# Kernel tuning notes

Measured on AMD Instinct MI355X. Metric: run time of the kernel, lower is better.

## Reference

```python
import jax, jax.numpy as jnp
import numpy as np
from jax import lax

B, T, H, E, V, ENC = 2048, 48, 512, 256, 128, 1024


def setup_inputs() -> dict:
    key = jax.random.key(0)
    ks = jax.random.split(key, 13)
    s = 0.05  # weight scale to keep activations sane
    return {
        "tgt_ids": jax.random.randint(ks[0], (B, T), 0, V),
        "enc_hid": jax.random.normal(ks[1], (B, ENC), jnp.float32),
        "W_init1": s * jax.random.normal(ks[2], (ENC, H), jnp.float32),
        "W_init2": s * jax.random.normal(ks[3], (ENC, H), jnp.float32),
        "embed_table": s * jax.random.normal(ks[4], (V, E), jnp.float32),
        "k1": s * jax.random.normal(ks[5], (E, 3 * H), jnp.float32),
        "rk1": s * jax.random.normal(ks[6], (H, 3 * H), jnp.float32),
        "b1": jnp.zeros((2, 3 * H), jnp.float32),
        "k2": s * jax.random.normal(ks[7], (H, 3 * H), jnp.float32),
        "rk2": s * jax.random.normal(ks[8], (H, 3 * H), jnp.float32),
        "b2": jnp.zeros((2, 3 * H), jnp.float32),
        "Wv": s * jax.random.normal(ks[9], (H, V), jnp.float32),
        "bv": jnp.zeros((V,), jnp.float32),
    }


def gru_masked(x_proj, mask, h0, rk, rb):
    """Keras GRU (reset_after=True, gate order z,r,h) with mask carry-through.
    x_proj: [B,T,3H] precomputed x@kernel + input_bias. mask: [B,T] bool.
    Masked steps keep previous state AND previous output (Keras masking semantics;
    GRU output == state)."""
    def step(h, inp):
        xg, m = inp  # xg: [B,3H], m: [B]
        inner = h @ rk + rb  # [B,3H]
        xz, xr, xh = jnp.split(xg, 3, axis=-1)
        rz, rr, rh = jnp.split(inner, 3, axis=-1)
        z = jax.nn.sigmoid(xz + rz)
        r = jax.nn.sigmoid(xr + rr)
        hh = jnp.tanh(xh + r * rh)
        h_new = z * h + (1.0 - z) * hh
        h = jnp.where(m[:, None], h_new, h)
        return h, h

    _, seq = lax.scan(step, h0, (x_proj.transpose(1, 0, 2), mask.T))
    return seq.transpose(1, 0, 2)  # [B,T,H]


def reference(tgt_ids, enc_hid, W_init1, W_init2, embed_table,
              k1, rk1, b1, k2, rk2, b2, Wv, bv):
    mask = tgt_ids != 0  # mask_zero=True
    emb = embed_table[tgt_ids]  # [B,T,E]
    h01 = enc_hid @ W_init1  # Dense no-bias init of layer-1 state
    h02 = enc_hid @ W_init2
    x1 = emb @ k1 + b1[0]  # [B,T,3H]
    seq1 = gru_masked(x1, mask, h01, rk1, b1[1])
    x2 = seq1 @ k2 + b2[0]
    seq2 = gru_masked(x2, mask, h02, rk2, b2[1])
    probs = jax.nn.softmax(seq2 @ Wv + bv, axis=-1)  # [B,T,V]
    return probs
```

## Files before the change

kernel.cpp:

```cpp
#include <hip/hip_runtime.h>
#include <hip/hip_bf16.h>
#include <math.h>

#define B_   2048
#define T_   48
#define H_   512
#define E_   256
#define V_   128
#define ENC_ 1024
#define H3_  1536
#define BH_  (B_ * H_)
#define NBLK_ 512

typedef __attribute__((ext_vector_type(8))) short bf16x8;
typedef __attribute__((ext_vector_type(4))) float f32x4;
typedef unsigned short ushort_t;

#if defined(__has_builtin)
#if __has_builtin(__builtin_amdgcn_global_load_lds)
#define HAVE_ASYNC 1
#endif
#endif
#ifndef HAVE_ASYNC
#define HAVE_ASYNC 0
#endif

__device__ __forceinline__ void stage16(const ushort_t* g, ushort_t* l, int lane)
{
#if HAVE_ASYNC
    __builtin_amdgcn_global_load_lds(
        (const __attribute__((address_space(1))) unsigned int*)g,
        (__attribute__((address_space(3))) unsigned int*)l, 16, 0, 0);
#else
    *(bf16x8*)(l + lane * 8) = *(const bf16x8*)g;
#endif
}

__device__ __forceinline__ float sigmoidf_(float x) { return 1.0f / (1.0f + expf(-x)); }

constexpr int BM = 64, BN = 64, BK = 16;

__global__ __launch_bounds__(256) void gemm_f32(
    const float* __restrict__ A, const float* __restrict__ Bm,
    const float* __restrict__ bias, float* __restrict__ C,
    int M, int N, int K)
{
    __shared__ float As[BK][BM + 4];
    __shared__ float Bs[BK][BN + 4];

    const int tid = threadIdx.x;
    const int bm = blockIdx.y * BM;
    const int bn = blockIdx.x * BN;
    const int tm = (tid >> 4) * 4;
    const int tn = (tid & 15) * 4;
    const int lmA = tid >> 2;
    const int lkA = (tid & 3) * 4;
    const int lkB = tid >> 4;
    const int lnB = (tid & 15) * 4;

    float acc[4][4] = {};

    for (int k0 = 0; k0 < K; k0 += BK) {
        float4 av  = *(const float4*)(A  + (size_t)(bm + lmA) * K + (k0 + lkA));
        float4 bv4 = *(const float4*)(Bm + (size_t)(k0 + lkB) * N + (bn + lnB));
        As[lkA + 0][lmA] = av.x;
        As[lkA + 1][lmA] = av.y;
        As[lkA + 2][lmA] = av.z;
        As[lkA + 3][lmA] = av.w;
        *(float4*)&Bs[lkB][lnB] = bv4;
        __syncthreads();

        #pragma unroll
        for (int k = 0; k < BK; ++k) {
            float4 a = *(const float4*)&As[k][tm];
            float4 b = *(const float4*)&Bs[k][tn];
            acc[0][0] += a.x * b.x; acc[0][1] += a.x * b.y; acc[0][2] += a.x * b.z; acc[0][3] += a.x * b.w;
            acc[1][0] += a.y * b.x; acc[1][1] += a.y * b.y; acc[1][2] += a.y * b.z; acc[1][3] += a.y * b.w;
            acc[2][0] += a.z * b.x; acc[2][1] += a.z * b.y; acc[2][2] += a.z * b.z; acc[2][3] += a.z * b.w;
            acc[3][0] += a.w * b.x; acc[3][1] += a.w * b.y; acc[3][2] += a.w * b.z; acc[3][3] += a.w * b.w;
        }
        __syncthreads();
    }

    #pragma unroll
    for (int r = 0; r < 4; ++r)
        #pragma unroll
        for (int c = 0; c < 4; ++c) {
            float v = acc[r][c];
            if (bias) v += bias[bn + tn + c];
            C[(size_t)(bm + tm + r) * N + (bn + tn + c)] = v;
        }
}

__global__ __launch_bounds__(256) void transpose_to_bf16(
    const float* __restrict__ W, __hip_bfloat16* __restrict__ Wt, int K, int N)
{
    __shared__ float tile[32][33];
    const int bk = blockIdx.y * 32, bn = blockIdx.x * 32;
    const int tx = threadIdx.x & 31, ty = threadIdx.x >> 5;
    #pragma unroll
    for (int i = ty; i < 32; i += 8)
        tile[i][tx] = W[(size_t)(bk + i) * N + (bn + tx)];
    __syncthreads();
    #pragma unroll
    for (int i = ty; i < 32; i += 8)
        Wt[(size_t)(bn + i) * K + (bk + tx)] = __float2bfloat16(tile[tx][i]);
}

__global__ __launch_bounds__(256) void transpose_split(
    const float* __restrict__ W, __hip_bfloat16* __restrict__ Whi,
    __hip_bfloat16* __restrict__ Wlo, int K, int N)
{
    __shared__ float tile[32][33];
    const int bk = blockIdx.y * 32, bn = blockIdx.x * 32;
    const int tx = threadIdx.x & 31, ty = threadIdx.x >> 5;
    #pragma unroll
    for (int i = ty; i < 32; i += 8)
        tile[i][tx] = W[(size_t)(bk + i) * N + (bn + tx)];
    __syncthreads();
    #pragma unroll
    for (int i = ty; i < 32; i += 8) {
        const float v = tile[tx][i];
        const __hip_bfloat16 h = __float2bfloat16(v);
        Whi[(size_t)(bn + i) * K + (bk + tx)] = h;
        Wlo[(size_t)(bn + i) * K + (bk + tx)] = __float2bfloat16(v - __bfloat162float(h));
    }
}

__global__ __launch_bounds__(256) void split_cast(
    const float* __restrict__ x, __hip_bfloat16* __restrict__ hi,
    __hip_bfloat16* __restrict__ lo, int n)
{
    const int i0 = (blockIdx.x * 256 + threadIdx.x) * 4;
    if (i0 >= n) return;
    const float4 v = *(const float4*)(x + i0);
    const float vv[4] = { v.x, v.y, v.z, v.w };
    #pragma unroll
    for (int j = 0; j < 4; ++j) {
        const __hip_bfloat16 h = __float2bfloat16(vv[j]);
        hi[i0 + j] = h;
        lo[i0 + j] = __float2bfloat16(vv[j] - __bfloat162float(h));
    }
}

__global__ __launch_bounds__(256, 2) void init_mfma(
    const ushort_t* __restrict__ ehi, const ushort_t* __restrict__ elo,
    const ushort_t* __restrict__ w1hi, const ushort_t* __restrict__ w1lo,
    const ushort_t* __restrict__ w2hi, const ushort_t* __restrict__ w2lo,
    float* __restrict__ h1f, __hip_bfloat16* __restrict__ h1b,
    float* __restrict__ h2f, __hip_bfloat16* __restrict__ h2b)
{
    const ushort_t* whi = blockIdx.z ? w2hi : w1hi;
    const ushort_t* wlo = blockIdx.z ? w2lo : w1lo;
    float* hf = blockIdx.z ? h2f : h1f;
    __hip_bfloat16* hb = blockIdx.z ? h2b : h1b;

    __shared__ __attribute__((aligned(16))) ushort_t Ahi[2][4096];
    __shared__ __attribute__((aligned(16))) ushort_t Alo[2][4096];
    __shared__ __attribute__((aligned(16))) ushort_t Bhi[2][2048];
    __shared__ __attribute__((aligned(16))) ushort_t Blo[2][2048];

    const int tid  = threadIdx.x;
    const int lane = tid & 63;
    const int w    = tid >> 6;
    const int ln   = lane & 15;
    const int kg   = lane >> 4;
    const int wr   = w >> 1, wc = w & 1;
    const int m0   = blockIdx.y * 64;
    const int i0   = blockIdx.x * 32;

    const int crow = lane >> 3;
    const int ckof = ((lane & 7) ^ crow) * 8;
    const int ko0 = (kg * 8) ^ ((ln & 7) * 8);
    const int ko1 = (32 + kg * 8) ^ ((ln & 7) * 8);

    auto STG = [&](int pb, int k0) {
        #pragma unroll
        for (int c = w; c < 24; c += 4) {
            const ushort_t* g; ushort_t* l;
            if (c < 8) {
                g = ehi + (size_t)(m0 + c * 8 + crow) * ENC_ + k0 + ckof;
                l = &Ahi[pb][c * 512];
            } else if (c < 16) {
                const int cc = c - 8;
                g = elo + (size_t)(m0 + cc * 8 + crow) * ENC_ + k0 + ckof;
                l = &Alo[pb][cc * 512];
            } else if (c < 20) {
                const int cc = c - 16;
                g = whi + (size_t)(i0 + cc * 8 + crow) * ENC_ + k0 + ckof;
                l = &Bhi[pb][cc * 512];
            } else {
                const int cc = c - 20;
                g = wlo + (size_t)(i0 + cc * 8 + crow) * ENC_ + k0 + ckof;
                l = &Blo[pb][cc * 512];
            }
            stage16(g, l, lane);
        }
    };

    f32x4 acc[2] = {};
    STG(0, 0);
    __syncthreads();
    int buf = 0;
    for (int k0 = 0; k0 < ENC_; k0 += 64) {
        if (k0 + 64 < ENC_) STG(buf ^ 1, k0 + 64);
        #pragma unroll
        for (int kk = 0; kk < 2; ++kk) {
            const int ko = kk ? ko1 : ko0;
            bf16x8 ah[2], al[2], bh, bl;
            #pragma unroll
            for (int fm = 0; fm < 2; ++fm) {
                ah[fm] = *(const bf16x8*)(&Ahi[buf][(wr * 32 + fm * 16 + ln) * 64 + ko]);
                al[fm] = *(const bf16x8*)(&Alo[buf][(wr * 32 + fm * 16 + ln) * 64 + ko]);
            }
            bh = *(const bf16x8*)(&Bhi[buf][(wc * 16 + ln) * 64 + ko]);
            bl = *(const bf16x8*)(&Blo[buf][(wc * 16 + ln) * 64 + ko]);
            #pragma unroll
            for (int fm = 0; fm < 2; ++fm) {
                acc[fm] = __builtin_amdgcn_mfma_f32_16x16x32_bf16(ah[fm], bh, acc[fm], 0, 0, 0);
                acc[fm] = __builtin_amdgcn_mfma_f32_16x16x32_bf16(al[fm], bh, acc[fm], 0, 0, 0);
                acc[fm] = __builtin_amdgcn_mfma_f32_16x16x32_bf16(ah[fm], bl, acc[fm], 0, 0, 0);
            }
        }
        __syncthreads();
        buf ^= 1;
    }

    const int i = i0 + wc * 16 + ln;
    #pragma unroll
    for (int fm = 0; fm < 2; ++fm)
        #pragma unroll
        for (int r = 0; r < 4; ++r) {
            const int b = m0 + wr * 32 + fm * 16 + kg * 4 + r;
            const float v = acc[fm][r];
            hf[(size_t)b * H_ + i] = v;
            hb[(size_t)b * H_ + i] = __float2bfloat16(v);
        }
}

__device__ __forceinline__ void l1_phase(
    ushort_t* Al0, ushort_t* Bl0,
    int lin, int t,
    const int* __restrict__ tgt, const float* __restrict__ xe1,
    const ushort_t* __restrict__ rkt, const float* __restrict__ rb,
    const float* __restrict__ hf_cur, const ushort_t* __restrict__ hb_cur,
    float* __restrict__ hf_nxt, __hip_bfloat16* __restrict__ hb_nxt)
{
    const int tid  = threadIdx.x;
    const int lane = tid & 63;
    const int w    = tid >> 6;
    const int ln   = lane & 15;
    const int kg   = lane >> 4;
    const int wr   = w >> 1, wc = w & 1;

    const int swz = (lin & 7) * 64 + (lin >> 3);
    const int m0  = (swz >> 4) * 64;
    const int i0  = (swz & 15) * 32;

    const int crow = lane >> 3;
    const int ckof = ((lane & 7) ^ crow) * 8;
    const int i    = i0 + wc * 16 + ln;

    const float rbz = rb[i], rbr = rb[H_ + i], rbh = rb[2 * H_ + i];
    int   ids[2][4];
    float hvs[2][4];
    #pragma unroll
    for (int fm = 0; fm < 2; ++fm)
        #pragma unroll
        for (int r = 0; r < 4; ++r) {
            const int b = m0 + wr * 32 + fm * 16 + kg * 4 + r;
            ids[fm][r] = tgt[(size_t)b * T_ + t];
            hvs[fm][r] = hf_cur[(size_t)b * H_ + i];
        }
    float xgz[2][4], xgr[2][4], xgh[2][4];
    #pragma unroll
    for (int fm = 0; fm < 2; ++fm)
        #pragma unroll
        for (int r = 0; r < 4; ++r) {
            const float* xg = xe1 + (size_t)ids[fm][r] * H3_;
            xgz[fm][r] = xg[i]; xgr[fm][r] = xg[H_ + i]; xgh[fm][r] = xg[2 * H_ + i];
        }

    const int ko0 = (kg * 8) ^ ((ln & 7) * 8);
    const int ko1 = (32 + kg * 8) ^ ((ln & 7) * 8);

    f32x4 acc[2][3] = {};

    auto STAGE = [&](int pb, int k0) {
        #pragma unroll
        for (int c = w; c < 20; c += 4) {
            const ushort_t* g; ushort_t* l;
            if (c < 8) {
                g = hb_cur + (size_t)(m0 + c * 8 + crow) * H_ + k0 + ckof;
                l = Al0 + pb * 4096 + c * 512;
            } else {
                const int idx = c - 8;
                g = rkt + (size_t)((idx >> 2) * H_ + i0 + (idx & 3) * 8 + crow) * H_ + k0 + ckof;
                l = Bl0 + pb * 6144 + idx * 512;
            }
            stage16(g, l, lane);
        }
    };

    STAGE(0, 0);
    __syncthreads();
    int buf = 0;
    for (int k0 = 0; k0 < H_; k0 += 64) {
        if (k0 + 64 < H_) STAGE(buf ^ 1, k0 + 64);
        #pragma unroll
        for (int kk = 0; kk < 2; ++kk) {
            const int ko = kk ? ko1 : ko0;
            bf16x8 af[2], bf[3];
            #pragma unroll
            for (int fm = 0; fm < 2; ++fm)
                af[fm] = *(const bf16x8*)(Al0 + buf * 4096 + (wr * 32 + fm * 16 + ln) * 64 + ko);
            #pragma unroll
            for (int g = 0; g < 3; ++g)
                bf[g] = *(const bf16x8*)(Bl0 + buf * 6144 + g * 2048 + (wc * 16 + ln) * 64 + ko);
            #pragma unroll
            for (int fm = 0; fm < 2; ++fm)
                #pragma unroll
                for (int g = 0; g < 3; ++g)
                    acc[fm][g] = __builtin_amdgcn_mfma_f32_16x16x32_bf16(
                        af[fm], bf[g], acc[fm][g], 0, 0, 0);
        }
        __syncthreads();
        buf ^= 1;
    }

    #pragma unroll
    for (int fm = 0; fm < 2; ++fm)
        #pragma unroll
        for (int r = 0; r < 4; ++r) {
            const int b = m0 + wr * 32 + fm * 16 + kg * 4 + r;
            const float hv = hvs[fm][r];
            float z  = sigmoidf_(xgz[fm][r] + acc[fm][0][r] + rbz);
            float rr = sigmoidf_(xgr[fm][r] + acc[fm][1][r] + rbr);
            float hh = tanhf(xgh[fm][r] + rr * (acc[fm][2][r] + rbh));
            float hn = (ids[fm][r] != 0) ? (z * hv + (1.0f - z) * hh) : hv;
            hf_nxt[(size_t)b * H_ + i] = hn;
            hb_nxt[(size_t)b * H_ + i] = __float2bfloat16(hn);
        }
}

__device__ __forceinline__ void l2_phase(
    ushort_t* lds, int lin, int t,
    const int* __restrict__ tgt,
    const ushort_t* __restrict__ k2t, const ushort_t* __restrict__ rk2t,
    const float* __restrict__ bx, const float* __restrict__ br,
    const ushort_t* __restrict__ s1b,
    const float* __restrict__ hf_cur,
    const ushort_t* __restrict__ hb_cur, size_t hbs,
    float* __restrict__ hf_nxt,
    __hip_bfloat16* __restrict__ hbo, size_t hos)
{
    ushort_t* A0l = lds;
    ushort_t* A1l = lds + 8192;
    ushort_t* B0l = lds + 16384;
    ushort_t* B1l = lds + 22528;

    const int tid  = threadIdx.x;
    const int lane = tid & 63;
    const int w    = tid >> 6;
    const int ln   = lane & 15;
    const int kg   = lane >> 4;
    const int wr   = w >> 1, wc = w & 1;

    const int swz = (lin & 7) * 64 + (lin >> 3);
    const int m0  = (swz >> 4) * 64;
    const int i0  = (swz & 15) * 32;

    const int crow = lane >> 3;
    const int ckof = ((lane & 7) ^ crow) * 8;
    const int i    = i0 + wc * 16 + ln;

    const float bxz = bx[i], bxr = bx[H_ + i], bxh = bx[2 * H_ + i];
    const float brz = br[i], brr = br[H_ + i], brh = br[2 * H_ + i];
    int   ids[2][4];
    float hvs[2][4];
    #pragma unroll
    for (int fm = 0; fm < 2; ++fm)
        #pragma unroll
        for (int r = 0; r < 4; ++r) {
            const int b = m0 + wr * 32 + fm * 16 + kg * 4 + r;
            ids[fm][r] = tgt[(size_t)b * T_ + t];
            hvs[fm][r] = hf_cur[(size_t)b * H_ + i];
        }

    const int ko0 = (kg * 8) ^ ((ln & 7) * 8);
    const int ko1 = (32 + kg * 8) ^ ((ln & 7) * 8);

    auto STAGE_A = [&](int pb, int k0) {
        #pragma unroll
        for (int c = w; c < 16; c += 4) {
            const ushort_t* g; ushort_t* l;
            if (c < 8) {
                g = s1b + (size_t)(m0 + c * 8 + crow) * H_ + k0 + ckof;
                l = A0l + pb * 4096 + c * 512;
            } else {
                const int cc = c - 8;
                g = hb_cur + (size_t)(m0 + cc * 8 + crow) * hbs + k0 + ckof;
                l = A1l + pb * 4096 + cc * 512;
            }
            stage16(g, l, lane);
        }
    };
    auto STAGE_B = [&](int k0) {
        #pragma unroll
        for (int c = w; c < 24; c += 4) {
            const ushort_t* g; ushort_t* l;
            if (c < 12) {
                g = k2t + (size_t)((c >> 2) * H_ + i0 + (c & 3) * 8 + crow) * H_ + k0 + ckof;
                l = B0l + c * 512;
            } else {
                const int idx = c - 12;
                g = rk2t + (size_t)((idx >> 2) * H_ + i0 + (idx & 3) * 8 + crow) * H_ + k0 + ckof;
                l = B1l + idx * 512;
            }
            stage16(g, l, lane);
        }
    };

    f32x4 acc0[2][3] = {};
    f32x4 acc1[2][3] = {};

    STAGE_A(0, 0);
    STAGE_B(0);
    __syncthreads();
    int buf = 0;
    for (int k0 = 0; k0 < H_; k0 += 64) {
        const bool more = (k0 + 64 < H_);
        if (more) STAGE_A(buf ^ 1, k0 + 64);

        bf16x8 a0f[2][2], a1f[2][2], b0f[2][3], b1f[2][3];
        #pragma unroll
        for (int kk = 0; kk < 2; ++kk) {
            const int ko = kk ? ko1 : ko0;
            #pragma unroll
            for (int fm = 0; fm < 2; ++fm) {
                a0f[kk][fm] = *(const bf16x8*)(A0l + buf * 4096 + (wr * 32 + fm * 16 + ln) * 64 + ko);
                a1f[kk][fm] = *(const bf16x8*)(A1l + buf * 4096 + (wr * 32 + fm * 16 + ln) * 64 + ko);
            }
            #pragma unroll
            for (int g = 0; g < 3; ++g) {
                b0f[kk][g] = *(const bf16x8*)(B0l + g * 2048 + (wc * 16 + ln) * 64 + ko);
                b1f[kk][g] = *(const bf16x8*)(B1l + g * 2048 + (wc * 16 + ln) * 64 + ko);
            }
        }
        __builtin_amdgcn_sched_barrier(0);
        asm volatile("s_waitcnt lgkmcnt(0)" ::: "memory");
        __builtin_amdgcn_sched_barrier(0);
        __builtin_amdgcn_s_barrier();
        if (more) STAGE_B(k0 + 64);

        #pragma unroll
        for (int kk = 0; kk < 2; ++kk)
            #pragma unroll
            for (int fm = 0; fm < 2; ++fm)
                #pragma unroll
                for (int g = 0; g < 3; ++g) {
                    acc0[fm][g] = __builtin_amdgcn_mfma_f32_16x16x32_bf16(
                        a0f[kk][fm], b0f[kk][g], acc0[fm][g], 0, 0, 0);
                    acc1[fm][g] = __builtin_amdgcn_mfma_f32_16x16x32_bf16(
                        a1f[kk][fm], b1f[kk][g], acc1[fm][g], 0, 0, 0);
                }
        __syncthreads();
        buf ^= 1;
    }

    #pragma unroll
    for (int fm = 0; fm < 2; ++fm)
        #pragma unroll
        for (int r = 0; r < 4; ++r) {
            const int b = m0 + wr * 32 + fm * 16 + kg * 4 + r;
            const float hv = hvs[fm][r];
            float z  = sigmoidf_((acc0[fm][0][r] + bxz) + (acc1[fm][0][r] + brz));
            float rr = sigmoidf_((acc0[fm][1][r] + bxr) + (acc1[fm][1][r] + brr));
            float hh = tanhf((acc0[fm][2][r] + bxh) + rr * (acc1[fm][2][r] + brh));
            float hn = (ids[fm][r] != 0) ? (z * hv + (1.0f - z) * hh) : hv;
            hf_nxt[(size_t)b * H_ + i] = hn;
            hbo[(size_t)b * hos + i] = __float2bfloat16(hn);
        }
}

__global__ __launch_bounds__(256, 2) void l1_fused(
    const int* __restrict__ tgt, int t,
    const float* __restrict__ xe1, const ushort_t* __restrict__ rkt,
    const float* __restrict__ rb,
    const float* __restrict__ hf_cur, const ushort_t* __restrict__ hb_cur,
    float* __restrict__ hf_nxt, __hip_bfloat16* __restrict__ hb_nxt)
{
    __shared__ __attribute__((aligned(16))) ushort_t lds[20480];
    l1_phase(lds, lds + 8192, blockIdx.x, t, tgt, xe1, rkt, rb,
             hf_cur, hb_cur, hf_nxt, hb_nxt);
}

__global__ __launch_bounds__(256, 2) void l2_fused(
    const int* __restrict__ tgt, int t,
    const ushort_t* __restrict__ k2t, const ushort_t* __restrict__ rk2t,
    const float* __restrict__ bx, const float* __restrict__ br,
    const ushort_t* __restrict__ s1b,
    const float* __restrict__ hf_cur,
    const ushort_t* __restrict__ hb_cur, size_t hbs,
    float* __restrict__ hf_nxt,
    __hip_bfloat16* __restrict__ hbo, size_t hos)
{
    __shared__ __attribute__((aligned(16))) ushort_t lds[28672];
    l2_phase(lds, blockIdx.x, t, tgt, k2t, rk2t, bx, br, s1b,
             hf_cur, hb_cur, hbs, hf_nxt, hbo, hos);
}

__device__ __forceinline__ void grid_barrier(unsigned* bar)
{
    __syncthreads();
    if (threadIdx.x == 0) {
        __threadfence();
        const unsigned g = __hip_atomic_load(&bar[1], __ATOMIC_RELAXED, __HIP_MEMORY_SCOPE_AGENT);
        const unsigned arrived =
            __hip_atomic_fetch_add(&bar[0], 1u, __ATOMIC_ACQ_REL, __HIP_MEMORY_SCOPE_AGENT) + 1u;
        if (arrived == (unsigned)NBLK_) {
            __hip_atomic_store(&bar[0], 0u, __ATOMIC_RELAXED, __HIP_MEMORY_SCOPE_AGENT);
            __hip_atomic_store(&bar[1], g + 1u, __ATOMIC_RELEASE, __HIP_MEMORY_SCOPE_AGENT);
        } else {
            while (__hip_atomic_load(&bar[1], __ATOMIC_ACQUIRE, __HIP_MEMORY_SCOPE_AGENT) == g)
                __builtin_amdgcn_s_sleep(2);
        }
        __threadfence();
    }
    __syncthreads();
}

__global__ __launch_bounds__(256, 2) void recurrence_all(
    const int* __restrict__ tgt, const float* __restrict__ xe1,
    const ushort_t* __restrict__ rk1t, const float* __restrict__ rb1,
    const ushort_t* __restrict__ k2t, const ushort_t* __restrict__ rk2t,
    const float* __restrict__ bx, const float* __restrict__ br,
    float* __restrict__ h1f, __hip_bfloat16* __restrict__ h1b,
    float* __restrict__ h2f, __hip_bfloat16* __restrict__ h2b,
    __hip_bfloat16* __restrict__ seq2b, unsigned* __restrict__ bar)
{
    __shared__ __attribute__((aligned(16))) ushort_t lds[28672];
    const int lin = blockIdx.x;

    #pragma unroll 1
    for (int t = 0; t < T_; ++t) {
        const int cur = t & 1, nxt = cur ^ 1;

        l1_phase(lds, lds + 8192, lin, t, tgt, xe1, rk1t, rb1,
                 h1f + (size_t)cur * BH_,
                 (const ushort_t*)(h1b + (size_t)cur * BH_),
                 h1f + (size_t)nxt * BH_,
                 h1b + (size_t)nxt * BH_);
        grid_barrier(bar);

        const ushort_t* hb_c = (t == 0)
            ? (const ushort_t*)h2b
            : (const ushort_t*)(seq2b + (size_t)(t - 1) * H_);
        const size_t hbs = (t == 0) ? (size_t)H_ : (size_t)T_ * H_;

        l2_phase(lds, lin, t, tgt, k2t, rk2t, bx, br,
                 (const ushort_t*)(h1b + (size_t)nxt * BH_),
                 h2f + (size_t)cur * BH_, hb_c, hbs,
                 h2f + (size_t)nxt * BH_,
                 seq2b + (size_t)t * H_, (size_t)T_ * H_);
        grid_barrier(bar);
    }
}

__device__ __forceinline__ void softmax_write4(
    float ax, float ay, float az, float aw, float* __restrict__ outp, int cg)
{
    float m = fmaxf(fmaxf(ax, ay), fmaxf(az, aw));
    #pragma unroll
    for (int d = 16; d >= 1; d >>= 1) m = fmaxf(m, __shfl_xor(m, d));
    float ex = __expf(ax - m), ey = __expf(ay - m),
          ez = __expf(az - m), ew = __expf(aw - m);
    float s = ex + ey + ez + ew;
    #pragma unroll
    for (int d = 16; d >= 1; d >>= 1) s += __shfl_xor(s, d);
    float inv = 1.0f / s;
    float4 o; o.x = ex * inv; o.y = ey * inv; o.z = ez * inv; o.w = ew * inv;
    *(float4*)(outp + cg * 4) = o;
}

__global__ __launch_bounds__(256) void out_softmax(
    const float* __restrict__ h2, const float* __restrict__ Wv,
    const float* __restrict__ bv, float* __restrict__ out, int t)
{
    const int tid = threadIdx.x;
    const int cg = tid & 31;
    const int rg = tid >> 5;
    const int row0 = blockIdx.x * 16;

    __shared__ float hs[16][512];
    for (int idx = tid; idx < 16 * 512; idx += 256)
        hs[idx >> 9][idx & 511] = h2[(size_t)(row0 + (idx >> 9)) * 512 + (idx & 511)];
    __syncthreads();

    const int r0 = rg * 2;
    const float4 bvv = *(const float4*)(bv + cg * 4);
    float a0x = bvv.x, a0y = bvv.y, a0z = bvv.z, a0w = bvv.w;
    float a1x = bvv.x, a1y = bvv.y, a1z = bvv.z, a1w = bvv.w;

    #pragma unroll 4
    for (int k = 0; k < 512; ++k) {
        float4 wv = *(const float4*)(Wv + (size_t)k * V_ + cg * 4);
        float h0 = hs[r0][k], h1 = hs[r0 + 1][k];
        a0x += h0 * wv.x; a0y += h0 * wv.y; a0z += h0 * wv.z; a0w += h0 * wv.w;
        a1x += h1 * wv.x; a1y += h1 * wv.y; a1z += h1 * wv.z; a1w += h1 * wv.w;
    }

    softmax_write4(a0x, a0y, a0z, a0w, out + ((size_t)(row0 + r0) * T_ + t) * V_, cg);
    softmax_write4(a1x, a1y, a1z, a1w, out + ((size_t)(row0 + r0 + 1) * T_ + t) * V_, cg);
}

__global__ __launch_bounds__(256) void proj_mfma(
    const ushort_t* __restrict__ s2, const ushort_t* __restrict__ wvt,
    const float* __restrict__ bv, float* __restrict__ out)
{
    const int lane = threadIdx.x & 63;
    const int w    = threadIdx.x >> 6;
    const int ln   = lane & 15;
    const int kg   = lane >> 4;
    const size_t row0 = (size_t)blockIdx.x * 128 + (size_t)w * 32;

    float bvl[8];
    #pragma unroll
    for (int nf = 0; nf < 8; ++nf) bvl[nf] = bv[nf * 16 + ln];

    f32x4 acc[2][8] = {};
    #pragma unroll 2
    for (int k0 = 0; k0 < H_; k0 += 32) {
        bf16x8 af[2], bf[8];
        #pragma unroll
        for (int mf = 0; mf < 2; ++mf)
            af[mf] = *(const bf16x8*)(s2 + (row0 + mf * 16 + ln) * H_ + k0 + kg * 8);
        #pragma unroll
        for (int nf = 0; nf < 8; ++nf)
            bf[nf] = *(const bf16x8*)(wvt + (size_t)(nf * 16 + ln) * H_ + k0 + kg * 8);
        #pragma unroll
        for (int mf = 0; mf < 2; ++mf)
            #pragma unroll
            for (int nf = 0; nf < 8; ++nf)
                acc[mf][nf] = __builtin_amdgcn_mfma_f32_16x16x32_bf16(
                    af[mf], bf[nf], acc[mf][nf], 0, 0, 0);
    }

    #pragma unroll
    for (int mf = 0; mf < 2; ++mf)
        #pragma unroll
        for (int q = 0; q < 4; ++q) {
            float v[8];
            float m = -1e30f;
            #pragma unroll
            for (int nf = 0; nf < 8; ++nf) { v[nf] = acc[mf][nf][q] + bvl[nf]; m = fmaxf(m, v[nf]); }
            #pragma unroll
            for (int d = 1; d <= 8; d <<= 1) m = fmaxf(m, __shfl_xor(m, d));
            float s = 0.f;
            #pragma unroll
            for (int nf = 0; nf < 8; ++nf) { v[nf] = __expf(v[nf] - m); s += v[nf]; }
            #pragma unroll
            for (int d = 1; d <= 8; d <<= 1) s += __shfl_xor(s, d);
            const float inv = 1.0f / s;
            float* op = out + (row0 + mf * 16 + kg * 4 + q) * V_;
            #pragma unroll
            for (int nf = 0; nf < 8; ++nf) op[nf * 16 + ln] = v[nf] * inv;
        }
}

extern "C" void kernel_launch(void* const* d_in, const int* in_sizes, int n_in,
                              void* d_out, int out_size, void* d_ws, size_t ws_size,
                              hipStream_t stream)
{
    const int*   tgt  = (const int*)  d_in[0];
    const float* enc  = (const float*)d_in[1];
    const float* Wi1  = (const float*)d_in[2];
    const float* Wi2  = (const float*)d_in[3];
    const float* emb  = (const float*)d_in[4];
    const float* k1   = (const float*)d_in[5];
    const float* rk1  = (const float*)d_in[6];
    const float* b1   = (const float*)d_in[7];
    const float* k2   = (const float*)d_in[8];
    const float* rk2  = (const float*)d_in[9];
    const float* b2   = (const float*)d_in[10];
    const float* Wv   = (const float*)d_in[11];
    const float* bv   = (const float*)d_in[12];
    float* out = (float*)d_out;

    float* ws  = (float*)d_ws;
    float* xe1 = ws;
    float* h1f = xe1 + (size_t)V_ * H3_;
    float* h2f = h1f + (size_t)2 * BH_;
    __hip_bfloat16* h1b = (__hip_bfloat16*)(h2f + (size_t)2 * BH_);
    __hip_bfloat16* h2b = h1b + (size_t)2 * BH_;
    __hip_bfloat16* rk1t = h2b + (size_t)2 * BH_;
    __hip_bfloat16* k2t  = rk1t + (size_t)H3_ * H_;
    __hip_bfloat16* rk2t = k2t  + (size_t)H3_ * H_;
    __hip_bfloat16* wvt  = rk2t + (size_t)H3_ * H_;
    __hip_bfloat16* ehi  = wvt + (size_t)V_ * H_;
    __hip_bfloat16* elo  = ehi + (size_t)B_ * ENC_;
    __hip_bfloat16* w1hi = elo + (size_t)B_ * ENC_;
    __hip_bfloat16* w1lo = w1hi + (size_t)H_ * ENC_;
    __hip_bfloat16* w2hi = w1lo + (size_t)H_ * ENC_;
    __hip_bfloat16* w2lo = w2hi + (size_t)H_ * ENC_;
    __hip_bfloat16* seq2b = w2lo + (size_t)H_ * ENC_;
    unsigned* bar = (unsigned*)(seq2b + (size_t)B_ * T_ * H_);

    const size_t need = (size_t)((char*)bar + 64 - (char*)d_ws);
    const bool batched = ws_size >= need;

    static int persist_state = -1;
    if (persist_state < 0) {
        int nb = 0;
        hipError_t e1 = hipOccupancyMaxActiveBlocksPerMultiprocessor(&nb, recurrence_all, 256, 0);
        hipDeviceProp_t prop;
        hipError_t e2 = hipGetDeviceProperties(&prop, 0);
        persist_state = (e1 == hipSuccess && e2 == hipSuccess &&
                         (long)nb * prop.multiProcessorCount >= NBLK_) ? 1 : 0;
    }
    const bool persist = batched && persist_state == 1;

    dim3 blk(256);

    transpose_to_bf16<<<dim3(H3_ / 32, H_ / 32), blk, 0, stream>>>(rk1, rk1t, H_, H3_);
    transpose_to_bf16<<<dim3(H3_ / 32, H_ / 32), blk, 0, stream>>>(k2,  k2t,  H_, H3_);
    transpose_to_bf16<<<dim3(H3_ / 32, H_ / 32), blk, 0, stream>>>(rk2, rk2t, H_, H3_);
    if (batched)
        transpose_to_bf16<<<dim3(V_ / 32, H_ / 32), blk, 0, stream>>>(Wv, wvt, H_, V_);

    split_cast<<<dim3((B_ * ENC_) / 1024), blk, 0, stream>>>(enc, ehi, elo, B_ * ENC_);
    transpose_split<<<dim3(H_ / 32, ENC_ / 32), blk, 0, stream>>>(Wi1, w1hi, w1lo, ENC_, H_);
    transpose_split<<<dim3(H_ / 32, ENC_ / 32), blk, 0, stream>>>(Wi2, w2hi, w2lo, ENC_, H_);

    gemm_f32<<<dim3(H3_ / BN, V_ / BM), blk, 0, stream>>>(emb, k1, b1, xe1, V_, H3_, E_);

    init_mfma<<<dim3(H_ / 32, B_ / 64, 2), blk, 0, stream>>>(
        (const ushort_t*)ehi, (const ushort_t*)elo,
        (const ushort_t*)w1hi, (const ushort_t*)w1lo,
        (const ushort_t*)w2hi, (const ushort_t*)w2lo,
        h1f, h1b, h2f, h2b);

    if (persist) {
        hipMemsetAsync(bar, 0, 64, stream);
        recurrence_all<<<dim3(NBLK_), blk, 0, stream>>>(
            tgt, xe1, (const ushort_t*)rk1t, b1 + H3_,
            (const ushort_t*)k2t, (const ushort_t*)rk2t, b2, b2 + H3_,
            h1f, h1b, h2f, h2b, seq2b, bar);
        proj_mfma<<<dim3((B_ * T_) / 128), blk, 0, stream>>>(
            (const ushort_t*)seq2b, (const ushort_t*)wvt, bv, out);
        return;
    }

    const dim3 fgrid(NBLK_);
    for (int t = 0; t < T_; ++t) {
        const int cur = t & 1, nxt = cur ^ 1;
        float* h1f_c = h1f + (size_t)cur * BH_;
        float* h1f_n = h1f + (size_t)nxt * BH_;
        float* h2f_c = h2f + (size_t)cur * BH_;
        float* h2f_n = h2f + (size_t)nxt * BH_;
        __hip_bfloat16* h1b_c = h1b + (size_t)cur * BH_;
        __hip_bfloat16* h1b_n = h1b + (size_t)nxt * BH_;

        l1_fused<<<fgrid, blk, 0, stream>>>(
            tgt, t, xe1, (const ushort_t*)rk1t, b1 + H3_,
            h1f_c, (const ushort_t*)h1b_c, h1f_n, h1b_n);

        const ushort_t* hb_c; size_t hbs;
        __hip_bfloat16* hbo; size_t hos;
        if (batched) {
            hb_c = (t == 0) ? (const ushort_t*)h2b
                            : (const ushort_t*)(seq2b + (size_t)(t - 1) * H_);
            hbs  = (t == 0) ? (size_t)H_ : (size_t)T_ * H_;
            hbo  = seq2b + (size_t)t * H_;
            hos  = (size_t)T_ * H_;
        } else {
            hb_c = (const ushort_t*)(h2b + (size_t)cur * BH_); hbs = H_;
            hbo  = h2b + (size_t)nxt * BH_;                    hos = H_;
        }

        l2_fused<<<fgrid, blk, 0, stream>>>(
            tgt, t, (const ushort_t*)k2t, (const ushort_t*)rk2t, b2, b2 + H3_,
            (const ushort_t*)h1b_n, h2f_c, hb_c, hbs, h2f_n, hbo, hos);

        if (!batched)
            out_softmax<<<dim3(B_ / 16), blk, 0, stream>>>(h2f_n, Wv, bv, out, t);
    }

    if (batched)
        proj_mfma<<<dim3((B_ * T_) / 128), blk, 0, stream>>>(
            (const ushort_t*)seq2b, (const ushort_t*)wvt, bv, out);
}
```

Before: 1.475 ms.

## Pair L2 step with next L1 step per barrier and keep fp32 state in registers

New measurement: 1.529 ms. 3.6% more time.

```diff
diff --git a/kernel.cpp b/kernel.cpp
--- a/kernel.cpp
+++ b/kernel.cpp
@@ -37,6 +37,12 @@
 }
 
 __device__ __forceinline__ float sigmoidf_(float x) { return 1.0f / (1.0f + expf(-x)); }
+
+__device__ __forceinline__ void tile_map(int lin, int& m0, int& i0)
+{
+    i0 = ((((lin & 7) << 1) | ((lin >> 3) & 1))) * 32;
+    m0 = (lin >> 4) * 64;
+}
 
 constexpr int BM = 64, BN = 64, BK = 16;
 
@@ -240,11 +246,13 @@
 
 __device__ __forceinline__ void l1_phase(
     ushort_t* Al0, ushort_t* Bl0,
-    int lin, int t,
+    int m0, int i0, int i, int t,
     const int* __restrict__ tgt, const float* __restrict__ xe1,
-    const ushort_t* __restrict__ rkt, const float* __restrict__ rb,
-    const float* __restrict__ hf_cur, const ushort_t* __restrict__ hb_cur,
-    float* __restrict__ hf_nxt, __hip_bfloat16* __restrict__ hb_nxt)
+    const ushort_t* __restrict__ rkt,
+    float rbz, float rbr, float rbh,
+    const ushort_t* __restrict__ hb_cur,
+    __hip_bfloat16* __restrict__ hb_nxt,
+    float (&hv)[2][4])
 {
     const int tid  = threadIdx.x;
     const int lane = tid & 63;
@@ -252,25 +260,18 @@
     const int ln   = lane & 15;
     const int kg   = lane >> 4;
     const int wr   = w >> 1, wc = w & 1;
-
-    const int swz = (lin & 7) * 64 + (lin >> 3);
-    const int m0  = (swz >> 4) * 64;
-    const int i0  = (swz & 15) * 32;
+    (void)wc;
 
     const int crow = lane >> 3;
     const int ckof = ((lane & 7) ^ crow) * 8;
-    const int i    = i0 + wc * 16 + ln;
-
-    const float rbz = rb[i], rbr = rb[H_ + i], rbh = rb[2 * H_ + i];
-    int   ids[2][4];
-    float hvs[2][4];
+
+    int ids[2][4];
     #pragma unroll
     for (int fm = 0; fm < 2; ++fm)
         #pragma unroll
         for (int r = 0; r < 4; ++r) {
             const int b = m0 + wr * 32 + fm * 16 + kg * 4 + r;
             ids[fm][r] = tgt[(size_t)b * T_ + t];
-            hvs[fm][r] = hf_cur[(size_t)b * H_ + i];
         }
     float xgz[2][4], xgr[2][4], xgh[2][4];
     #pragma unroll
@@ -316,7 +317,7 @@
                 af[fm] = *(const bf16x8*)(Al0 + buf * 4096 + (wr * 32 + fm * 16 + ln) * 64 + ko);
             #pragma unroll
             for (int g = 0; g < 3; ++g)
-                bf[g] = *(const bf16x8*)(Bl0 + buf * 6144 + g * 2048 + (wc * 16 + ln) * 64 + ko);
+                bf[g] = *(const bf16x8*)(Bl0 + buf * 6144 + g * 2048 + ((w & 1) * 16 + ln) * 64 + ko);
             #pragma unroll
             for (int fm = 0; fm < 2; ++fm)
                 #pragma unroll
@@ -333,26 +334,27 @@
         #pragma unroll
         for (int r = 0; r < 4; ++r) {
             const int b = m0 + wr * 32 + fm * 16 + kg * 4 + r;
-            const float hv = hvs[fm][r];
+            const float hvv = hv[fm][r];
             float z  = sigmoidf_(xgz[fm][r] + acc[fm][0][r] + rbz);
             float rr = sigmoidf_(xgr[fm][r] + acc[fm][1][r] + rbr);
             float hh = tanhf(xgh[fm][r] + rr * (acc[fm][2][r] + rbh));
-            float hn = (ids[fm][r] != 0) ? (z * hv + (1.0f - z) * hh) : hv;
-            hf_nxt[(size_t)b * H_ + i] = hn;
+            float hn = (ids[fm][r] != 0) ? (z * hvv + (1.0f - z) * hh) : hvv;
+            hv[fm][r] = hn;
             hb_nxt[(size_t)b * H_ + i] = __float2bfloat16(hn);
         }
 }
 
 __device__ __forceinline__ void l2_phase(
-    ushort_t* lds, int lin, int t,
+    ushort_t* lds,
+    int m0, int i0, int i, int t,
     const int* __restrict__ tgt,
     const ushort_t* __restrict__ k2t, const ushort_t* __restrict__ rk2t,
-    const float* __restrict__ bx, const float* __restrict__ br,
+    float bxz, float bxr, float bxh,
+    float brz, float brr, float brh,
     const ushort_t* __restrict__ s1b,
-    const float* __restrict__ hf_cur,
-    const ushort_t* __restrict__ hb_cur, size_t hbs,
-    float* __restrict__ hf_nxt,
-    __hip_bfloat16* __restrict__ hbo, size_t hos)
+    const ushort_t* __restrict__ a1, size_t a1s,
+    __hip_bfloat16* __restrict__ hbo, size_t hos,
+    float (&hv)[2][4])
 {
     ushort_t* A0l = lds;
     ushort_t* A1l = lds + 8192;
@@ -365,26 +367,18 @@
     const int ln   = lane & 15;
     const int kg   = lane >> 4;
     const int wr   = w >> 1, wc = w & 1;
-
-    const int swz = (lin & 7) * 64 + (lin >> 3);
-    const int m0  = (swz >> 4) * 64;
-    const int i0  = (swz & 15) * 32;
+    (void)wc;
 
     const int crow = lane >> 3;
     const int ckof = ((lane & 7) ^ crow) * 8;
-    const int i    = i0 + wc * 16 + ln;
-
-    const float bxz = bx[i], bxr = bx[H_ + i], bxh = bx[2 * H_ + i];
-    const float brz = br[i], brr = br[H_ + i], brh = br[2 * H_ + i];
-    int   ids[2][4];
-    float hvs[2][4];
+
+    int ids[2][4];
     #pragma unroll
     for (int fm = 0; fm < 2; ++fm)
         #pragma unroll
         for (int r = 0; r < 4; ++r) {
             const int b = m0 + wr * 32 + fm * 16 + kg * 4 + r;
             ids[fm][r] = tgt[(size_t)b * T_ + t];
-            hvs[fm][r] = hf_cur[(size_t)b * H_ + i];
         }
 
     const int ko0 = (kg * 8) ^ ((ln & 7) * 8);
@@ -399,7 +393,7 @@
                 l = A0l + pb * 4096 + c * 512;
             } else {
                 const int cc = c - 8;
-                g = hb_cur + (size_t)(m0 + cc * 8 + crow) * hbs + k0 + ckof;
+                g = a1 + (size_t)(m0 + cc * 8 + crow) * a1s + k0 + ckof;
                 l = A1l + pb * 4096 + cc * 512;
             }
             stage16(g, l, lane);
@@ -443,8 +437,8 @@
             }
             #pragma unroll
             for (int g = 0; g < 3; ++g) {
-                b0f[kk][g] = *(const bf16x8*)(B0l + g * 2048 + (wc * 16 + ln) * 64 + ko);
-                b1f[kk][g] = *(const bf16x8*)(B1l + g * 2048 + (wc * 16 + ln) * 64 + ko);
+                b0f[kk][g] = *(const bf16x8*)(B0l + g * 2048 + ((w & 1) * 16 + ln) * 64 + ko);
+                b1f[kk][g] = *(const bf16x8*)(B1l + g * 2048 + ((w & 1) * 16 + ln) * 64 + ko);
             }
         }
         __builtin_amdgcn_sched_barrier(0);
@@ -473,12 +467,12 @@
         #pragma unroll
         for (int r = 0; r < 4; ++r) {
             const int b = m0 + wr * 32 + fm * 16 + kg * 4 + r;
-            const float hv = hvs[fm][r];
+            const float hvv = hv[fm][r];
             float z  = sigmoidf_((acc0[fm][0][r] + bxz) + (acc1[fm][0][r] + brz));
             float rr = sigmoidf_((acc0[fm][1][r] + bxr) + (acc1[fm][1][r] + brr));
             float hh = tanhf((acc0[fm][2][r] + bxh) + rr * (acc1[fm][2][r] + brh));
-            float hn = (ids[fm][r] != 0) ? (z * hv + (1.0f - z) * hh) : hv;
-            hf_nxt[(size_t)b * H_ + i] = hn;
+            float hn = (ids[fm][r] != 0) ? (z * hvv + (1.0f - z) * hh) : hvv;
+            hv[fm][r] = hn;
             hbo[(size_t)b * hos + i] = __float2bfloat16(hn);
         }
 }
@@ -491,8 +485,26 @@
     float* __restrict__ hf_nxt, __hip_bfloat16* __restrict__ hb_nxt)
 {
     __shared__ __attribute__((aligned(16))) ushort_t lds[20480];
-    l1_phase(lds, lds + 8192, blockIdx.x, t, tgt, xe1, rkt, rb,
-             hf_cur, hb_cur, hf_nxt, hb_nxt);
+    int m0, i0; tile_map(blockIdx.x, m0, i0);
+    const int tid = threadIdx.x, lane = tid & 63, w = tid >> 6;
+    const int ln = lane & 15, kg = lane >> 4, wr = w >> 1, wc = w & 1;
+    const int i = i0 + wc * 16 + ln;
+
+    float hv[2][4];
+    #pragma unroll
+    for (int fm = 0; fm < 2; ++fm)
+        #pragma unroll
+        for (int r = 0; r < 4; ++r)
+            hv[fm][r] = hf_cur[(size_t)(m0 + wr * 32 + fm * 16 + kg * 4 + r) * H_ + i];
+
+    l1_phase(lds, lds + 8192, m0, i0, i, t, tgt, xe1, rkt,
+             rb[i], rb[H_ + i], rb[2 * H_ + i], hb_cur, hb_nxt, hv);
+
+    #pragma unroll
+    for (int fm = 0; fm < 2; ++fm)
+        #pragma unroll
+        for (int r = 0; r < 4; ++r)
+            hf_nxt[(size_t)(m0 + wr * 32 + fm * 16 + kg * 4 + r) * H_ + i] = hv[fm][r];
 }
 
 __global__ __launch_bounds__(256, 2) void l2_fused(
@@ -506,8 +518,28 @@
     __hip_bfloat16* __restrict__ hbo, size_t hos)
 {
     __shared__ __attribute__((aligned(16))) ushort_t lds[28672];
-    l2_phase(lds, blockIdx.x, t, tgt, k2t, rk2t, bx, br, s1b,
-             hf_cur, hb_cur, hbs, hf_nxt, hbo, hos);
+    int m0, i0; tile_map(blockIdx.x, m0, i0);
+    const int tid = threadIdx.x, lane = tid & 63, w = tid >> 6;
+    const int ln = lane & 15, kg = lane >> 4, wr = w >> 1, wc = w & 1;
+    const int i = i0 + wc * 16 + ln;
+
+    float hv[2][4];
+    #pragma unroll
+    for (int fm = 0; fm < 2; ++fm)
+        #pragma unroll
+        for (int r = 0; r < 4; ++r)
+            hv[fm][r] = hf_cur[(size_t)(m0 + wr * 32 + fm * 16 + kg * 4 + r) * H_ + i];
+
+    l2_phase(lds, m0, i0, i, t, tgt, k2t, rk2t,
+             bx[i], bx[H_ + i], bx[2 * H_ + i],
+             br[i], br[H_ + i], br[2 * H_ + i],
+             s1b, hb_cur, hbs, hbo, hos, hv);
+
+    #pragma unroll
+    for (int fm = 0; fm < 2; ++fm)
+        #pragma unroll
+        for (int r = 0; r < 4; ++r)
+            hf_nxt[(size_t)(m0 + wr * 32 + fm * 16 + kg * 4 + r) * H_ + i] = hv[fm][r];
 }
 
 __device__ __forceinline__ void grid_barrier(unsigned* bar)
@@ -535,34 +567,53 @@
     const ushort_t* __restrict__ rk1t, const float* __restrict__ rb1,
     const ushort_t* __restrict__ k2t, const ushort_t* __restrict__ rk2t,
     const float* __restrict__ bx, const float* __restrict__ br,
-    float* __restrict__ h1f, __hip_bfloat16* __restrict__ h1b,
-    float* __restrict__ h2f, __hip_bfloat16* __restrict__ h2b,
+    const float* __restrict__ h1f0, __hip_bfloat16* __restrict__ h1b,
+    const float* __restrict__ h2f0, const __hip_bfloat16* __restrict__ h2b0,
     __hip_bfloat16* __restrict__ seq2b, unsigned* __restrict__ bar)
 {
     __shared__ __attribute__((aligned(16))) ushort_t lds[28672];
-    const int lin = blockIdx.x;
+    int m0, i0; tile_map(blockIdx.x, m0, i0);
+    const int tid = threadIdx.x, lane = tid & 63, w = tid >> 6;
+    const int ln = lane & 15, kg = lane >> 4, wr = w >> 1, wc = w & 1;
+    const int i = i0 + wc * 16 + ln;
+
+    const float rbz = rb1[i], rbr = rb1[H_ + i], rbh = rb1[2 * H_ + i];
+    const float bxz = bx[i],  bxr = bx[H_ + i],  bxh = bx[2 * H_ + i];
+    const float brz = br[i],  brr = br[H_ + i],  brh = br[2 * H_ + i];
+
+    float hv1[2][4], hv2[2][4];
+    #pragma unroll
+    for (int fm = 0; fm < 2; ++fm)
+        #pragma unroll
+        for (int r = 0; r < 4; ++r) {
+            const size_t b = (size_t)(m0 + wr * 32 + fm * 16 + kg * 4 + r) * H_ + i;
+            hv1[fm][r] = h1f0[b];
+            hv2[fm][r] = h2f0[b];
+        }
+
+    l1_phase(lds, lds + 8192, m0, i0, i, 0, tgt, xe1, rk1t, rbz, rbr, rbh,
+             (const ushort_t*)h1b, h1b + BH_, hv1);
+    grid_barrier(bar);
 
     #pragma unroll 1
-    for (int t = 0; t < T_; ++t) {
-        const int cur = t & 1, nxt = cur ^ 1;
-
-        l1_phase(lds, lds + 8192, lin, t, tgt, xe1, rk1t, rb1,
-                 h1f + (size_t)cur * BH_,
-                 (const ushort_t*)(h1b + (size_t)cur * BH_),
-                 h1f + (size_t)nxt * BH_,
-                 h1b + (size_t)nxt * BH_);
-        grid_barrier(bar);
-
-        const ushort_t* hb_c = (t == 0)
-            ? (const ushort_t*)h2b
-            : (const ushort_t*)(seq2b + (size_t)(t - 1) * H_);
-        const size_t hbs = (t == 0) ? (size_t)H_ : (size_t)T_ * H_;
-
-        l2_phase(lds, lin, t, tgt, k2t, rk2t, bx, br,
-                 (const ushort_t*)(h1b + (size_t)nxt * BH_),
-                 h2f + (size_t)cur * BH_, hb_c, hbs,
-                 h2f + (size_t)nxt * BH_,
-                 seq2b + (size_t)t * H_, (size_t)T_ * H_);
+    for (int p = 0; p < T_; ++p) {
+        const ushort_t* a1 = (p == 0)
+            ? (const ushort_t*)h2b0
+            : (const ushort_t*)(seq2b + (size_t)(p - 1) * H_);
+        const size_t a1s = (p == 0) ? (size_t)H_ : (size_t)T_ * H_;
+        const ushort_t* s1 = (const ushort_t*)(h1b + (size_t)((p + 1) & 1) * BH_);
+
+        l2_phase(lds, m0, i0, i, p, tgt, k2t, rk2t,
+                 bxz, bxr, bxh, brz, brr, brh,
+                 s1, a1, a1s,
+                 seq2b + (size_t)p * H_, (size_t)T_ * H_, hv2);
+
+        if (p + 1 < T_)
+            l1_phase(lds, lds + 8192, m0, i0, i, p + 1, tgt, xe1, rk1t,
+                     rbz, rbr, rbh,
+                     (const ushort_t*)(h1b + (size_t)((p + 1) & 1) * BH_),
+                     h1b + (size_t)((p + 2) & 1) * BH_, hv1);
+
         grid_barrier(bar);
     }
 }
```
